# Optimization experiments

Measured on AMD Instinct MI355X. Metric: run time of the kernel, lower is better.

Reference implementation:

```python
import jax, jax.numpy as jnp
import numpy as np

N = 50000      # nodes
E = 1_600_000  # edges (avg degree 32)
G = 2000       # graphs in batch
H = 2          # attention heads
C = 64         # out_channels
IN = 64        # in_channels
NEG_SLOPE = 0.2


def setup_inputs() -> dict:
    key = jax.random.key(0)
    ks = jax.random.split(key, 6)
    x = jax.random.normal(ks[0], (N, IN), dtype=jnp.float32)
    edge_index = jax.random.randint(ks[1], (2, E), 0, N, dtype=jnp.int32)
    batch = jnp.sort(jax.random.randint(ks[2], (N,), 0, G, dtype=jnp.int32))
    # GATConv params: lin weight [H*C, IN] (glorot-ish), att vectors, bias [C]
    W = jax.random.normal(ks[3], (H * C, IN), dtype=jnp.float32) * (1.0 / np.sqrt(IN))
    att_src = jax.random.normal(ks[4], (1, H, C), dtype=jnp.float32) * 0.1
    att_dst = jax.random.normal(ks[5], (1, H, C), dtype=jnp.float32) * 0.1
    bias = jnp.zeros((C,), dtype=jnp.float32)
    return {"x": x, "edge_index": edge_index, "batch": batch,
            "W": W, "att_src": att_src, "att_dst": att_dst, "bias": bias}


def reference(x, edge_index, batch, W, att_src, att_dst, bias):
    # --- GATConv (PyG semantics: add_self_loops=True, concat=False -> head mean + bias) ---
    loops = jnp.arange(N, dtype=edge_index.dtype)
    src = jnp.concatenate([edge_index[0], loops])  # [E+N]
    dst = jnp.concatenate([edge_index[1], loops])  # [E+N]

    xp = (x @ W.T).reshape(N, H, C)                 # projected node feats [N,H,C]
    a_src = jnp.sum(xp * att_src, axis=-1)          # [N,H]
    a_dst = jnp.sum(xp * att_dst, axis=-1)          # [N,H]

    e = jax.nn.leaky_relu(a_src[src] + a_dst[dst], NEG_SLOPE)  # [E+N,H]
    # segment softmax over incoming edges of each destination node
    m = jax.ops.segment_max(e, dst, num_segments=N)            # [N,H]
    e = jnp.exp(e - m[dst])
    s = jax.ops.segment_sum(e, dst, num_segments=N)            # [N,H]
    alpha = e / s[dst]                                         # [E+N,H]

    msg = xp[src] * alpha[:, :, None]                          # [E+N,H,C]
    out = jax.ops.segment_sum(msg, dst, num_segments=N)        # [N,H,C]
    h_nodes = out.mean(axis=1) + bias                          # [N,C]

    # --- global_mean_pool ---
    sums = jax.ops.segment_sum(h_nodes, batch, num_segments=G)                     # [G,C]
    cnt = jax.ops.segment_sum(jnp.ones((N, 1), h_nodes.dtype), batch, num_segments=G)
    h_graphs = sums / jnp.maximum(cnt, 1.0)                                        # [G,C]
    return (h_nodes, h_graphs)
```

## Files before the change

kernel.cpp:

```cpp
#include <hip/hip_runtime.h>
#include <hip/hip_bf16.h>

#define H 2
#define C 64
#define IN_CH 64
#define HC (H*C)
#define NEG_SLOPE 0.2f
#define NBUCK_MAX 512
#define SBLK 512
#define CAP 6144

__global__ __launch_bounds__(128) void proj_kernel(
    const float* __restrict__ x, const float* __restrict__ W,
    const float* __restrict__ att_src, const float* __restrict__ att_dst,
    const int* __restrict__ batch, __hip_bfloat16* __restrict__ xp,
    float* __restrict__ asrc, float* __restrict__ adst, int* __restrict__ cnt,
    int* __restrict__ gbeg, int N, int nbuck, int G) {
    int t = threadIdx.x;
    if (blockIdx.x == 0)
        for (int i = t; i < nbuck; i += 128) cnt[i] = 0;
    {
        int i = blockIdx.x * 128 + t;
        if (i < N) {
            int bi = batch[i];
            if (i == 0) {
                for (int g = 0; g <= bi; g++) gbeg[g] = 0;
            } else {
                int bp = batch[i - 1];
                for (int g = bp + 1; g <= bi; g++) gbeg[g] = i;
            }
            if (i == N - 1)
                for (int g = bi + 1; g <= G; g++) gbeg[g] = N;
        }
    }
    float w[64];
    const float4* wr = reinterpret_cast<const float4*>(W + (size_t)t * IN_CH);
#pragma unroll
    for (int q = 0; q < 16; q++) {
        float4 v = wr[q];
        w[4 * q] = v.x; w[4 * q + 1] = v.y; w[4 * q + 2] = v.z; w[4 * q + 3] = v.w;
    }
    float a_s = att_src[t], a_d = att_dst[t];
    int lane = t & 63, head = t >> 6;
    for (int n = blockIdx.x; n < N; n += gridDim.x) {
        const float* xr = x + (size_t)n * IN_CH;
        float acc = 0.f;
#pragma unroll
        for (int k = 0; k < 64; k++) acc = fmaf(w[k], xr[k], acc);
        xp[(size_t)n * HC + t] = __float2bfloat16(acc);
        float as = acc * a_s, ad = acc * a_d;
#pragma unroll
        for (int d = 32; d > 0; d >>= 1) {
            as += __shfl_xor(as, d, 64);
            ad += __shfl_xor(ad, d, 64);
        }
        if (lane == 0) {
            asrc[(size_t)n * H + head] = as;
            adst[(size_t)n * H + head] = ad;
        }
    }
}

__global__ __launch_bounds__(256) void scatter_kernel(
    const int* __restrict__ edge, int* __restrict__ cnt,
    int* __restrict__ staged, int N, int E) {
    const int tid = threadIdx.x, bid = blockIdx.x;
    const int nbuck = (N + 127) >> 7;
    const int chunkE = (E + SBLK - 1) / SBLK;
    const int* srcE = edge;
    const int* dstE = edge + E;
    __shared__ int lh[NBUCK_MAX], bse[NBUCK_MAX], lcur[NBUCK_MAX];
    for (int i = tid; i < nbuck; i += 256) { lh[i] = 0; lcur[i] = 0; }
    __syncthreads();
    int beg = bid * chunkE, end = min(beg + chunkE, E);
    for (int i = beg + tid; i < end; i += 256)
        atomicAdd(&lh[dstE[i] >> 7], 1);
    __syncthreads();
    for (int i = tid; i < nbuck; i += 256)
        bse[i] = atomicAdd(&cnt[i], lh[i]);
    __syncthreads();
    for (int i = beg + tid; i < end; i += 256) {
        int s = srcE[i], d = dstE[i];
        int b = d >> 7;
        int l = atomicAdd(&lcur[b], 1);
        staged[(size_t)b * CAP + bse[b] + l] = s | ((d & 127) << 20);
    }
}

__global__ __launch_bounds__(512) void bucket_csr_kernel(
    const int* __restrict__ staged, const int* __restrict__ cnt,
    int* __restrict__ off, int* __restrict__ csr, int N, int nbuck) {
    int b = blockIdx.x, t = threadIdx.x;
    __shared__ int bse[512], rs[512], lh[128], sh[128], cur[128];
    {
        int v = (t < nbuck) ? cnt[t] : 0;
        bse[t] = v; rs[t] = v;
        __syncthreads();
        for (int d = 1; d < 512; d <<= 1) {
            int u = (t >= d) ? bse[t - d] : 0;
            __syncthreads();
            bse[t] += u;
            __syncthreads();
        }
        bse[t] -= rs[t];
        __syncthreads();
    }
    int base = bse[b], size = rs[b];
    const int* st = staged + (size_t)b * CAP;
    if (t < 128) lh[t] = 0;
    __syncthreads();
    for (int i = t; i < size; i += 512)
        atomicAdd(&lh[st[i] >> 20], 1);
    __syncthreads();
    int v = (t < 128) ? lh[t] : 0;
    if (t < 128) sh[t] = v;
    __syncthreads();
    for (int d = 1; d < 128; d <<= 1) {
        int u = (t >= d && t < 128) ? sh[t - d] : 0;
        __syncthreads();
        if (t < 128) sh[t] += u;
        __syncthreads();
    }
    if (t < 128) {
        int ex = sh[t] - v;
        int nd = b * 128 + t;
        if (nd < N) off[nd] = base + ex;
        if (nd == N - 1) off[N] = base + size;
        cur[t] = base + ex;
    }
    __syncthreads();
    for (int i = t; i < size; i += 512) {
        int e = st[i];
        int pos = atomicAdd(&cur[e >> 20], 1);
        csr[pos] = e & 0xFFFFF;
    }
}

template<int NB>
__device__ __forceinline__ void gfma(const uint* __restrict__ xpw,
                                     const int* __restrict__ si,
                                     const float* __restrict__ swl,
                                     uint laneoff, float& accx, float& accy) {
    const char* xb = reinterpret_cast<const char*>(xpw);
    uint bu[NB];
#pragma unroll
    for (int j = 0; j < NB; j++) {
        uint boff = (uint)si[j] + laneoff;
        bu[j] = *reinterpret_cast<const uint*>(xb + boff);
    }
#pragma unroll
    for (int j = 0; j < NB; j++) {
        float w = swl[2 * j];
        accx = fmaf(w, __uint_as_float(bu[j] << 16), accx);
        accy = fmaf(w, __uint_as_float(bu[j] & 0xffff0000u), accy);
    }
}

__global__ __launch_bounds__(256, 4) void aggregate_kernel(
    const __hip_bfloat16* __restrict__ xp, const float* __restrict__ asrc,
    const float* __restrict__ adst, const int* __restrict__ off,
    const int* __restrict__ csr, const float* __restrict__ bias,
    float* __restrict__ out, int N) {
    __shared__ int sidx[4][32];
    __shared__ float swf[4][64];
    int wid = threadIdx.x >> 6;
    int n = blockIdx.x * 4 + wid;
    if (n >= N) return;
    int lane = threadIdx.x & 63;
    int cl = lane & 31;
    int hsel = lane >> 5;
    int* si = sidx[wid];
    float* swl = swf[wid] + hsel;
    int o0 = off[n];
    int deg = off[n + 1] - o0;
    float adh = adst[2 * n + hsel];
    float es = asrc[2 * n + hsel] + adh;
    es = (es > 0.f) ? es : NEG_SLOPE * es;
    float wself = __expf(es);
    float ssum = (cl == 0) ? wself : 0.f;

    const uint* xpw = reinterpret_cast<const uint*>(xp);
    uint laneoff = (uint)lane * 4u;
    float accx, accy;
    {
        uint u = xpw[(size_t)n * 64 + lane];
        accx = wself * __uint_as_float(u << 16);
        accy = wself * __uint_as_float(u & 0xffff0000u);
    }

    for (int base = 0; base < deg; base += 32) {
        int i = base + cl;
        int idx = 0;
        float w = 0.f;
        if (i < deg) {
            idx = csr[o0 + i];
            float t = asrc[2 * idx + hsel] + adh;
            t = (t > 0.f) ? t : NEG_SLOPE * t;
            w = __expf(t);
        }
        ssum += w;
        if (!hsel) si[cl] = idx << 8;
        swl[2 * cl] = w;
        int nb = min(deg - base, 32);
        if (nb > 16) gfma<32>(xpw, si, swl, laneoff, accx, accy);
        else         gfma<16>(xpw, si, swl, laneoff, accx, accy);
    }
#pragma unroll
    for (int d = 16; d > 0; d >>= 1) ssum += __shfl_xor(ssum, d, 64);
    float inv = 1.f / ssum;
    accx *= inv;
    accy *= inv;
    float ox = 0.5f * (accx + __shfl_xor(accx, 32, 64));
    float oy = 0.5f * (accy + __shfl_xor(accy, 32, 64));
    if (lane < 32) {
        float vx = ox + bias[2 * cl];
        float vy = oy + bias[2 * cl + 1];
        *reinterpret_cast<float2*>(out + (size_t)n * C + 2 * cl) = make_float2(vx, vy);
    }
}

__global__ __launch_bounds__(256) void pool_kernel(const float* __restrict__ hn,
                                                   const int* __restrict__ gbeg,
                                                   float* __restrict__ outG, int G) {
    int g = blockIdx.x;
    int c = threadIdx.x & 63, r = threadIdx.x >> 6;
    int beg = gbeg[g], end = gbeg[g + 1];
    float s = 0.f;
    for (int n = beg + r; n < end; n += 4) s += hn[(size_t)n * C + c];
    __shared__ float red[256];
    red[threadIdx.x] = s;
    __syncthreads();
    if (r == 0) {
        float tot = red[c] + red[64 + c] + red[128 + c] + red[192 + c];
        outG[(size_t)g * C + c] = tot / fmaxf((float)(end - beg), 1.f);
    }
}

extern "C" void kernel_launch(void* const* d_in, const int* in_sizes, int n_in,
                              void* d_out, int out_size, void* d_ws, size_t ws_size,
                              hipStream_t stream) {
    const float* x       = (const float*)d_in[0];
    const int*   edge    = (const int*)d_in[1];
    const int*   batch   = (const int*)d_in[2];
    const float* W       = (const float*)d_in[3];
    const float* att_src = (const float*)d_in[4];
    const float* att_dst = (const float*)d_in[5];
    const float* bias    = (const float*)d_in[6];

    int N = in_sizes[0] / IN_CH;
    int E = in_sizes[1] / 2;
    int G = out_size / C - N;
    int nbuck = (N + 127) >> 7;

    char* p = (char*)d_ws;
    auto alloc = [&](size_t bytes) {
        char* r = p;
        p += (bytes + 255) & ~(size_t)255;
        return r;
    };
    __hip_bfloat16* xp = (__hip_bfloat16*)alloc((size_t)N * HC * 2);
    float* asrc    = (float*)alloc((size_t)N * H * 4);
    float* adst    = (float*)alloc((size_t)N * H * 4);
    int*   cnt     = (int*)alloc((size_t)nbuck * 4);
    int*   off     = (int*)alloc((size_t)(N + 1) * 4);
    int*   staged  = (int*)alloc((size_t)nbuck * CAP * 4);
    int*   csr     = (int*)alloc((size_t)E * 4);
    int*   gbeg    = (int*)alloc((size_t)(G + 1) * 4);

    proj_kernel<<<2048, 128, 0, stream>>>(x, W, att_src, att_dst, batch, xp, asrc, adst,
                                          cnt, gbeg, N, nbuck, G);
    scatter_kernel<<<SBLK, 256, 0, stream>>>(edge, cnt, staged, N, E);
    bucket_csr_kernel<<<nbuck, 512, 0, stream>>>(staged, cnt, off, csr, N, nbuck);
    aggregate_kernel<<<(N + 3) / 4, 256, 0, stream>>>(xp, asrc, adst, off, csr, bias,
                                                      (float*)d_out, N);
    pool_kernel<<<G, 256, 0, stream>>>((const float*)d_out, gbeg,
                                       (float*)d_out + (size_t)N * C, G);
}
```

Before: 200.6 us.

## Fuse edge histogram into projection kernel and compute deterministic bucket bases

Moves the per-block destination-bucket histogram out of the scatter kernel and into extra blocks of the projection kernel, so the histogram pass overlaps with the dense projection work. A new prefix kernel scans per-block histograms into per-bucket, per-block base offsets, which replaces global atomicAdd reservations. The scatter kernel then only reads the precomputed bases and writes staged edges. This adds a kernel launch and extra histogram/base buffers in exchange for removing one edge pass and the global atomics from the scatter step.

New measurement: 199.8 us. About the same (-0.4%).

```diff
diff --git a/kernel.cpp b/kernel.cpp
--- a/kernel.cpp
+++ b/kernel.cpp
@@ -10,17 +10,32 @@
 #define SBLK 512
 #define CAP 6144
 
-__global__ __launch_bounds__(128) void proj_kernel(
+__global__ __launch_bounds__(128) void proj_hist_kernel(
     const float* __restrict__ x, const float* __restrict__ W,
     const float* __restrict__ att_src, const float* __restrict__ att_dst,
-    const int* __restrict__ batch, __hip_bfloat16* __restrict__ xp,
-    float* __restrict__ asrc, float* __restrict__ adst, int* __restrict__ cnt,
-    int* __restrict__ gbeg, int N, int nbuck, int G) {
+    const int* __restrict__ batch, const int* __restrict__ edge,
+    __hip_bfloat16* __restrict__ xp,
+    float* __restrict__ asrc, float* __restrict__ adst, int* __restrict__ hist,
+    int* __restrict__ gbeg, int N, int E, int G, int nbuck) {
     int t = threadIdx.x;
-    if (blockIdx.x == 0)
-        for (int i = t; i < nbuck; i += 128) cnt[i] = 0;
+    if (blockIdx.x < SBLK) {
+        __shared__ int lh[NBUCK_MAX];
+        for (int i = t; i < nbuck; i += 128) lh[i] = 0;
+        __syncthreads();
+        const int* dstE = edge + E;
+        int chunkE = (E + SBLK - 1) / SBLK;
+        int beg = blockIdx.x * chunkE, end = min(beg + chunkE, E);
+        for (int i = beg + t; i < end; i += 128)
+            atomicAdd(&lh[dstE[i] >> 7], 1);
+        __syncthreads();
+        for (int i = t; i < nbuck; i += 128)
+            hist[(size_t)blockIdx.x * nbuck + i] = lh[i];
+        return;
+    }
+    int pb = blockIdx.x - SBLK;
+    int gridP = gridDim.x - SBLK;
     {
-        int i = blockIdx.x * 128 + t;
+        int i = pb * 128 + t;
         if (i < N) {
             int bi = batch[i];
             if (i == 0) {
@@ -42,7 +57,7 @@
     }
     float a_s = att_src[t], a_d = att_dst[t];
     int lane = t & 63, head = t >> 6;
-    for (int n = blockIdx.x; n < N; n += gridDim.x) {
+    for (int n = pb; n < N; n += gridP) {
         const float* xr = x + (size_t)n * IN_CH;
         float acc = 0.f;
 #pragma unroll
@@ -61,29 +76,45 @@
     }
 }
 
+__global__ __launch_bounds__(512) void prefix_kernel(const int* __restrict__ hist,
+                                                     int* __restrict__ bse_t,
+                                                     int* __restrict__ cnt, int nbuck) {
+    int b = blockIdx.x;
+    int t = threadIdx.x;
+    __shared__ int sh[512];
+    int v = hist[(size_t)t * nbuck + b];
+    sh[t] = v;
+    __syncthreads();
+    for (int d = 1; d < 512; d <<= 1) {
+        int u = (t >= d) ? sh[t - d] : 0;
+        __syncthreads();
+        sh[t] += u;
+        __syncthreads();
+    }
+    bse_t[(size_t)b * SBLK + t] = sh[t] - v;
+    if (t == 511) cnt[b] = sh[511];
+}
+
 __global__ __launch_bounds__(256) void scatter_kernel(
-    const int* __restrict__ edge, int* __restrict__ cnt,
+    const int* __restrict__ edge, const int* __restrict__ bse_t,
     int* __restrict__ staged, int N, int E) {
     const int tid = threadIdx.x, bid = blockIdx.x;
     const int nbuck = (N + 127) >> 7;
     const int chunkE = (E + SBLK - 1) / SBLK;
     const int* srcE = edge;
     const int* dstE = edge + E;
-    __shared__ int lh[NBUCK_MAX], bse[NBUCK_MAX], lcur[NBUCK_MAX];
-    for (int i = tid; i < nbuck; i += 256) { lh[i] = 0; lcur[i] = 0; }
+    __shared__ int sbase[NBUCK_MAX], lcur[NBUCK_MAX];
+    for (int i = tid; i < nbuck; i += 256) {
+        sbase[i] = bse_t[(size_t)i * SBLK + bid];
+        lcur[i] = 0;
+    }
     __syncthreads();
     int beg = bid * chunkE, end = min(beg + chunkE, E);
-    for (int i = beg + tid; i < end; i += 256)
-        atomicAdd(&lh[dstE[i] >> 7], 1);
-    __syncthreads();
-    for (int i = tid; i < nbuck; i += 256)
-        bse[i] = atomicAdd(&cnt[i], lh[i]);
-    __syncthreads();
     for (int i = beg + tid; i < end; i += 256) {
         int s = srcE[i], d = dstE[i];
         int b = d >> 7;
         int l = atomicAdd(&lcur[b], 1);
-        staged[(size_t)b * CAP + bse[b] + l] = s | ((d & 127) << 20);
+        staged[(size_t)b * CAP + sbase[b] + l] = s | ((d & 127) << 20);
     }
 }
 
@@ -261,15 +292,19 @@
     __hip_bfloat16* xp = (__hip_bfloat16*)alloc((size_t)N * HC * 2);
     float* asrc    = (float*)alloc((size_t)N * H * 4);
     float* adst    = (float*)alloc((size_t)N * H * 4);
+    int*   hist    = (int*)alloc((size_t)SBLK * nbuck * 4);
+    int*   bse_t   = (int*)alloc((size_t)nbuck * SBLK * 4);
     int*   cnt     = (int*)alloc((size_t)nbuck * 4);
     int*   off     = (int*)alloc((size_t)(N + 1) * 4);
     int*   staged  = (int*)alloc((size_t)nbuck * CAP * 4);
     int*   csr     = (int*)alloc((size_t)E * 4);
     int*   gbeg    = (int*)alloc((size_t)(G + 1) * 4);
 
-    proj_kernel<<<2048, 128, 0, stream>>>(x, W, att_src, att_dst, batch, xp, asrc, adst,
-                                          cnt, gbeg, N, nbuck, G);
-    scatter_kernel<<<SBLK, 256, 0, stream>>>(edge, cnt, staged, N, E);
+    proj_hist_kernel<<<SBLK + 2048, 128, 0, stream>>>(x, W, att_src, att_dst, batch,
+                                                      edge, xp, asrc, adst, hist, gbeg,
+                                                      N, E, G, nbuck);
+    prefix_kernel<<<nbuck, 512, 0, stream>>>(hist, bse_t, cnt, nbuck);
+    scatter_kernel<<<SBLK, 256, 0, stream>>>(edge, bse_t, staged, N, E);
     bucket_csr_kernel<<<nbuck, 512, 0, stream>>>(staged, cnt, off, csr, N, nbuck);
     aggregate_kernel<<<(N + 3) / 4, 256, 0, stream>>>(xp, asrc, adst, off, csr, bias,
                                                       (float*)d_out, N);
```

## Fuse bucket CSR build into aggregation using shared-memory local CSR per bucket

Applied to the files above, without the earlier changes.

Removes the separate bucket_csr kernel and global CSR/offset arrays; each aggregation block now sorts its 64-node bucket's staged edges into shared memory and then aggregates those nodes, four waves handling 16 nodes each. Bucket size shrinks from 128 to 64 nodes so the 3072-entry local CSR fits in LDS. This drops a kernel launch and a global write/read of the CSR, but cuts the grid to about 782 blocks with a 12KB+ LDS footprint, which lowers parallelism and occupancy, and makes load balance depend on per-bucket degree. CAP 3072 must hold the largest bucket, which is only true for random graphs with average degree 32.

After: 203.8 us. About the same (+1.6%).

```diff
diff --git a/kernel.cpp b/kernel.cpp
--- a/kernel.cpp
+++ b/kernel.cpp
@@ -6,9 +6,10 @@
 #define IN_CH 64
 #define HC (H*C)
 #define NEG_SLOPE 0.2f
-#define NBUCK_MAX 512
+#define NBUCK_MAX 1024
 #define SBLK 512
-#define CAP 6144
+#define BKT 64
+#define CAP 3072
 
 __global__ __launch_bounds__(128) void proj_kernel(
     const float* __restrict__ x, const float* __restrict__ W,
@@ -65,7 +66,7 @@
     const int* __restrict__ edge, int* __restrict__ cnt,
     int* __restrict__ staged, int N, int E) {
     const int tid = threadIdx.x, bid = blockIdx.x;
-    const int nbuck = (N + 127) >> 7;
+    const int nbuck = (N + BKT - 1) / BKT;
     const int chunkE = (E + SBLK - 1) / SBLK;
     const int* srcE = edge;
     const int* dstE = edge + E;
@@ -74,74 +75,24 @@
     __syncthreads();
     int beg = bid * chunkE, end = min(beg + chunkE, E);
     for (int i = beg + tid; i < end; i += 256)
-        atomicAdd(&lh[dstE[i] >> 7], 1);
+        atomicAdd(&lh[dstE[i] >> 6], 1);
     __syncthreads();
     for (int i = tid; i < nbuck; i += 256)
         bse[i] = atomicAdd(&cnt[i], lh[i]);
     __syncthreads();
     for (int i = beg + tid; i < end; i += 256) {
         int s = srcE[i], d = dstE[i];
-        int b = d >> 7;
+        int b = d >> 6;
         int l = atomicAdd(&lcur[b], 1);
-        staged[(size_t)b * CAP + bse[b] + l] = s | ((d & 127) << 20);
-    }
-}
-
-__global__ __launch_bounds__(512) void bucket_csr_kernel(
-    const int* __restrict__ staged, const int* __restrict__ cnt,
-    int* __restrict__ off, int* __restrict__ csr, int N, int nbuck) {
-    int b = blockIdx.x, t = threadIdx.x;
-    __shared__ int bse[512], rs[512], lh[128], sh[128], cur[128];
-    {
-        int v = (t < nbuck) ? cnt[t] : 0;
-        bse[t] = v; rs[t] = v;
-        __syncthreads();
-        for (int d = 1; d < 512; d <<= 1) {
-            int u = (t >= d) ? bse[t - d] : 0;
-            __syncthreads();
-            bse[t] += u;
-            __syncthreads();
-        }
-        bse[t] -= rs[t];
-        __syncthreads();
-    }
-    int base = bse[b], size = rs[b];
-    const int* st = staged + (size_t)b * CAP;
-    if (t < 128) lh[t] = 0;
-    __syncthreads();
-    for (int i = t; i < size; i += 512)
-        atomicAdd(&lh[st[i] >> 20], 1);
-    __syncthreads();
-    int v = (t < 128) ? lh[t] : 0;
-    if (t < 128) sh[t] = v;
-    __syncthreads();
-    for (int d = 1; d < 128; d <<= 1) {
-        int u = (t >= d && t < 128) ? sh[t - d] : 0;
-        __syncthreads();
-        if (t < 128) sh[t] += u;
-        __syncthreads();
-    }
-    if (t < 128) {
-        int ex = sh[t] - v;
-        int nd = b * 128 + t;
-        if (nd < N) off[nd] = base + ex;
-        if (nd == N - 1) off[N] = base + size;
-        cur[t] = base + ex;
-    }
-    __syncthreads();
-    for (int i = t; i < size; i += 512) {
-        int e = st[i];
-        int pos = atomicAdd(&cur[e >> 20], 1);
-        csr[pos] = e & 0xFFFFF;
+        staged[(size_t)b * CAP + bse[b] + l] = s | ((d & 63) << 20);
     }
 }
 
 template<int NB>
-__device__ __forceinline__ void gfma(const uint* __restrict__ xpw,
+__device__ __forceinline__ void gfma(const char* __restrict__ xb,
                                      const int* __restrict__ si,
                                      const float* __restrict__ swl,
                                      uint laneoff, float& accx, float& accy) {
-    const char* xb = reinterpret_cast<const char*>(xpw);
     uint bu[NB];
 #pragma unroll
     for (int j = 0; j < NB; j++) {
@@ -156,66 +107,94 @@
     }
 }
 
-__global__ __launch_bounds__(256, 4) void aggregate_kernel(
+__global__ __launch_bounds__(256, 4) void csragg_kernel(
     const __hip_bfloat16* __restrict__ xp, const float* __restrict__ asrc,
-    const float* __restrict__ adst, const int* __restrict__ off,
-    const int* __restrict__ csr, const float* __restrict__ bias,
+    const float* __restrict__ adst, const int* __restrict__ cnt,
+    const int* __restrict__ staged_all, const float* __restrict__ bias,
     float* __restrict__ out, int N) {
+    __shared__ int lcsr[CAP];
+    __shared__ int loff[BKT + 1];
+    __shared__ int lh[BKT], cur[BKT];
     __shared__ int sidx[4][32];
     __shared__ float swf[4][64];
-    int wid = threadIdx.x >> 6;
-    int n = blockIdx.x * 4 + wid;
-    if (n >= N) return;
-    int lane = threadIdx.x & 63;
-    int cl = lane & 31;
-    int hsel = lane >> 5;
+    int b = blockIdx.x, tid = threadIdx.x;
+    int lane = tid & 63, wid = tid >> 6;
+    int size = cnt[b];
+    const int* st = staged_all + (size_t)b * CAP;
+    if (tid < BKT) lh[tid] = 0;
+    __syncthreads();
+    for (int i = tid; i < size; i += 256)
+        atomicAdd(&lh[st[i] >> 20], 1);
+    __syncthreads();
+    if (wid == 0) {
+        int v = lh[lane];
+        int inc = v;
+#pragma unroll
+        for (int d = 1; d < 64; d <<= 1) {
+            int u = __shfl_up(inc, d, 64);
+            if (lane >= d) inc += u;
+        }
+        loff[lane] = inc - v;
+        cur[lane] = inc - v;
+        if (lane == 63) loff[BKT] = inc;
+    }
+    __syncthreads();
+    for (int i = tid; i < size; i += 256) {
+        int e = st[i];
+        int pos = atomicAdd(&cur[e >> 20], 1);
+        lcsr[pos] = (e & 0xFFFFF) << 8;
+    }
+    __syncthreads();
+    const uint* xpw = reinterpret_cast<const uint*>(xp);
+    const char* xb = reinterpret_cast<const char*>(xp);
+    int cl = lane & 31, hsel = lane >> 5;
+    uint laneoff = (uint)lane * 4u;
     int* si = sidx[wid];
     float* swl = swf[wid] + hsel;
-    int o0 = off[n];
-    int deg = off[n + 1] - o0;
-    float adh = adst[2 * n + hsel];
-    float es = asrc[2 * n + hsel] + adh;
-    es = (es > 0.f) ? es : NEG_SLOPE * es;
-    float wself = __expf(es);
-    float ssum = (cl == 0) ? wself : 0.f;
-
-    const uint* xpw = reinterpret_cast<const uint*>(xp);
-    uint laneoff = (uint)lane * 4u;
-    float accx, accy;
-    {
+    for (int k = 0; k < 16; k++) {
+        int nd = wid * 16 + k;
+        int n = b * BKT + nd;
+        if (n >= N) break;
+        int o0 = loff[nd];
+        int deg = loff[nd + 1] - o0;
+        float adh = adst[2 * n + hsel];
+        float es = asrc[2 * n + hsel] + adh;
+        es = (es > 0.f) ? es : NEG_SLOPE * es;
+        float wself = __expf(es);
+        float ssum = (cl == 0) ? wself : 0.f;
         uint u = xpw[(size_t)n * 64 + lane];
-        accx = wself * __uint_as_float(u << 16);
-        accy = wself * __uint_as_float(u & 0xffff0000u);
-    }
-
-    for (int base = 0; base < deg; base += 32) {
-        int i = base + cl;
-        int idx = 0;
-        float w = 0.f;
-        if (i < deg) {
-            idx = csr[o0 + i];
-            float t = asrc[2 * idx + hsel] + adh;
-            t = (t > 0.f) ? t : NEG_SLOPE * t;
-            w = __expf(t);
-        }
-        ssum += w;
-        if (!hsel) si[cl] = idx << 8;
-        swl[2 * cl] = w;
-        int nb = min(deg - base, 32);
-        if (nb > 16) gfma<32>(xpw, si, swl, laneoff, accx, accy);
-        else         gfma<16>(xpw, si, swl, laneoff, accx, accy);
-    }
-#pragma unroll
-    for (int d = 16; d > 0; d >>= 1) ssum += __shfl_xor(ssum, d, 64);
-    float inv = 1.f / ssum;
-    accx *= inv;
-    accy *= inv;
-    float ox = 0.5f * (accx + __shfl_xor(accx, 32, 64));
-    float oy = 0.5f * (accy + __shfl_xor(accy, 32, 64));
-    if (lane < 32) {
-        float vx = ox + bias[2 * cl];
-        float vy = oy + bias[2 * cl + 1];
-        *reinterpret_cast<float2*>(out + (size_t)n * C + 2 * cl) = make_float2(vx, vy);
+        float accx = wself * __uint_as_float(u << 16);
+        float accy = wself * __uint_as_float(u & 0xffff0000u);
+        for (int base = 0; base < deg; base += 32) {
+            int i = base + cl;
+            int boff = 0;
+            float w = 0.f;
+            if (i < deg) {
+                boff = lcsr[o0 + i];
+                float t = asrc[(boff >> 7) + hsel] + adh;
+                t = (t > 0.f) ? t : NEG_SLOPE * t;
+                w = __expf(t);
+            }
+            ssum += w;
+            if (!hsel) si[cl] = boff;
+            swl[2 * cl] = w;
+            int nb = min(deg - base, 32);
+            if (nb > 16) gfma<32>(xb, si, swl, laneoff, accx, accy);
+            else         gfma<16>(xb, si, swl, laneoff, accx, accy);
+        }
+#pragma unroll
+        for (int d = 16; d > 0; d >>= 1) ssum += __shfl_xor(ssum, d, 64);
+        float inv = 1.f / ssum;
+        accx *= inv;
+        accy *= inv;
+        float ox = 0.5f * (accx + __shfl_xor(accx, 32, 64));
+        float oy = 0.5f * (accy + __shfl_xor(accy, 32, 64));
+        if (lane < 32) {
+            float vx = ox + bias[2 * cl];
+            float vy = oy + bias[2 * cl + 1];
+            *reinterpret_cast<float2*>(out + (size_t)n * C + 2 * cl) =
+                make_float2(vx, vy);
+        }
     }
 }
 
@@ -250,7 +229,7 @@
     int N = in_sizes[0] / IN_CH;
     int E = in_sizes[1] / 2;
     int G = out_size / C - N;
-    int nbuck = (N + 127) >> 7;
+    int nbuck = (N + BKT - 1) / BKT;
 
     char* p = (char*)d_ws;
     auto alloc = [&](size_t bytes) {
@@ -262,17 +241,14 @@
     float* asrc    = (float*)alloc((size_t)N * H * 4);
     float* adst    = (float*)alloc((size_t)N * H * 4);
     int*   cnt     = (int*)alloc((size_t)nbuck * 4);
-    int*   off     = (int*)alloc((size_t)(N + 1) * 4);
     int*   staged  = (int*)alloc((size_t)nbuck * CAP * 4);
-    int*   csr     = (int*)alloc((size_t)E * 4);
     int*   gbeg    = (int*)alloc((size_t)(G + 1) * 4);
 
     proj_kernel<<<2048, 128, 0, stream>>>(x, W, att_src, att_dst, batch, xp, asrc, adst,
                                           cnt, gbeg, N, nbuck, G);
     scatter_kernel<<<SBLK, 256, 0, stream>>>(edge, cnt, staged, N, E);
-    bucket_csr_kernel<<<nbuck, 512, 0, stream>>>(staged, cnt, off, csr, N, nbuck);
-    aggregate_kernel<<<(N + 3) / 4, 256, 0, stream>>>(xp, asrc, adst, off, csr, bias,
-                                                      (float*)d_out, N);
+    csragg_kernel<<<nbuck, 256, 0, stream>>>(xp, asrc, adst, cnt, staged, bias,
+                                             (float*)d_out, N);
     pool_kernel<<<G, 256, 0, stream>>>((const float*)d_out, gbeg,
                                        (float*)d_out + (size_t)N * C, G);
 }
```
